# Performance work log

Hardware: AMD Instinct MI355X
Metric: run time of the kernel (lower is better)

Reference implementation:

```python
import jax, jax.numpy as jnp
import numpy as np

B, L = 8, 1024
VOCAB = 5000
DW = 256            # d_word_vec = d_model
H = 3 * DW          # hidden_size = 768
NH, HD = 12, 64     # n_head, d_k
D = NH * HD         # 768 = nhead*head_dim
D_INNER = 3072
N_LAYERS = 2
N_HIDDEN = 1024
N_OUT = 5000
MASK = 0
SCALE = 1.0 / float(np.sqrt(HD))


def _sinusoid(n_pos, d_hid):
    pos = np.arange(n_pos, dtype=np.float64)[:, None]
    hid = np.arange(d_hid)[None, :]
    tab = pos / np.power(10000.0, 2 * (hid // 2) / d_hid)
    tab[:, 0::2] = np.sin(tab[:, 0::2])
    tab[:, 1::2] = np.cos(tab[:, 1::2])
    tab[0] = 0.0  # padding_idx=0
    return jnp.asarray(tab, dtype=jnp.float32)


def _ln(x, g, b, eps=1e-5):
    mu = x.mean(-1, keepdims=True)
    var = ((x - mu) ** 2).mean(-1, keepdims=True)
    return (x - mu) * jax.lax.rsqrt(var + eps) * g + b


def _dense(x, w, b):
    # w: [out, in] (torch Conv 1x1 / Linear convention)
    return jnp.einsum('...i,oi->...o', x, w) + b


def _pwff(x, w1, b1, w2, b2, g, bn):
    out = _dense(jax.nn.relu(_dense(x, w1, b1)), w2, b2)
    return _ln(out + x, g, bn)


def _msa1(x, relay, wq, bq, wk, bk, wv, bv, wo, bo):
    # x: [B, L, H] nodes, relay: [B, H]. Star-Transformer ring attention:
    # window = 3 local neighbors + the relay node (4 keys per query).
    Bx, Lx, _ = x.shape
    q = _dense(x, wq, bq).reshape(Bx, Lx, NH, HD)
    k = _dense(x, wk, bk).reshape(Bx, Lx, NH, HD)
    v = _dense(x, wv, bv).reshape(Bx, Lx, NH, HD)
    kp = jnp.pad(k, ((0, 0), (1, 1), (0, 0), (0, 0)))
    vp = jnp.pad(v, ((0, 0), (1, 1), (0, 0), (0, 0)))
    k_win = jnp.stack([kp[:, u:u + Lx] for u in range(3)], axis=2)  # [B,L,3,NH,HD]
    v_win = jnp.stack([vp[:, u:u + Lx] for u in range(3)], axis=2)
    rk = _dense(relay, wk, bk).reshape(Bx, NH, HD)
    rv = _dense(relay, wv, bv).reshape(Bx, NH, HD)
    s_loc = jnp.einsum('blnh,blwnh->blwn', q, k_win)
    s_rel = jnp.einsum('blnh,bnh->bln', q, rk)
    scores = jnp.concatenate([s_loc, s_rel[:, :, None, :]], axis=2) * SCALE  # [B,L,4,NH]
    a = jax.nn.softmax(scores, axis=2)
    att = jnp.einsum('blwn,blwnh->blnh', a[:, :, :3], v_win) + a[:, :, 3][..., None] * rv[:, None]
    return _dense(att.reshape(Bx, Lx, D), wo, bo)


def _msa2(relay, nodes, smask, wq, bq, wk, bk, wv, bv, wo, bo):
    # Satellite->planet global attention: single query (relay) over [relay; nodes].
    Bx = relay.shape[0]
    y = jnp.concatenate([relay[:, None, :], nodes], axis=1)  # [B, 1+L, H]
    q = _dense(relay, wq, bq).reshape(Bx, NH, HD)
    k = _dense(y, wk, bk).reshape(Bx, -1, NH, HD)
    v = _dense(y, wv, bv).reshape(Bx, -1, NH, HD)
    pre = jnp.einsum('bnh,bsnh->bns', q, k) * SCALE
    pre = jnp.where(smask[:, None, :], -jnp.inf, pre)
    a = jax.nn.softmax(pre, axis=2)
    att = jnp.einsum('bns,bsnh->bnh', a, v).reshape(Bx, D)
    return _dense(att, wo, bo)


def setup_inputs():
    ks = iter(jax.random.split(jax.random.key(0), 40))
    def w(shape):
        return jax.random.normal(next(ks), shape, dtype=jnp.float32) * 0.02
    def z(shape):
        return jnp.zeros(shape, jnp.float32)
    def o(shape):
        return jnp.ones(shape, jnp.float32)
    inp = {}
    inp['src_seq'] = jax.random.randint(next(ks), (B, L, 3), 0, VOCAB, dtype=jnp.int32)
    inp['positions'] = jax.random.randint(next(ks), (B,), 0, L, dtype=jnp.int32)
    inp['emb'] = w((VOCAB, DW))
    inp['pos_table'] = _sinusoid(L, H)
    inp['norm_g'] = o((N_LAYERS, H)); inp['norm_b'] = z((N_LAYERS, H))
    inp['pw_w1'] = w((N_LAYERS, D_INNER, H)); inp['pw_b1'] = z((N_LAYERS, D_INNER))
    inp['pw_w2'] = w((N_LAYERS, H, D_INNER)); inp['pw_b2'] = z((N_LAYERS, H))
    inp['pw_g'] = o((N_LAYERS, H)); inp['pw_bn'] = z((N_LAYERS, H))
    for p in ['ring', 'star']:
        inp[p + '_wq'] = w((N_LAYERS, D, H)); inp[p + '_bq'] = z((N_LAYERS, D))
        inp[p + '_wk'] = w((N_LAYERS, D, H)); inp[p + '_bk'] = z((N_LAYERS, D))
        inp[p + '_wv'] = w((N_LAYERS, D, H)); inp[p + '_bv'] = z((N_LAYERS, D))
        inp[p + '_wo'] = w((N_LAYERS, H, D)); inp[p + '_bo'] = z((N_LAYERS, H))
    inp['head_w1'] = w((3, N_HIDDEN, 2 * H)); inp['head_b1'] = z((3, N_HIDDEN))
    inp['head_w2'] = w((3, N_OUT, N_HIDDEN)); inp['head_b2'] = z((3, N_OUT))
    return inp


def reference(src_seq, positions, emb, pos_table, norm_g, norm_b, pw_w1, pw_b1, pw_w2, pw_b2, pw_g, pw_bn, ring_wq, ring_bq, ring_wk, ring_bk, ring_wv, ring_bv, ring_wo, ring_bo, star_wq, star_bq, star_wk, star_bk, star_wv, star_bv, star_wo, star_bo, head_w1, head_b1, head_w2, head_b2):
    Bx, Lx, _ = src_seq.shape
    # [B,L,3,DW] -> [B,L,H], add (frozen) sinusoid positional encoding
    x = emb[src_seq].reshape(Bx, Lx, H) + pos_table[None, :Lx]
    mask_pad = src_seq[:, :, 0] == MASK               # True at padded positions
    smask = jnp.concatenate([jnp.zeros((Bx, 1), bool), mask_pad], axis=1)
    nodes = x
    relay = x.mean(axis=1)                            # [B, H]
    for i in range(N_LAYERS):
        h = _pwff(nodes, pw_w1[i], pw_b1[i], pw_w2[i], pw_b2[i], pw_g[i], pw_bn[i])
        ring = _msa1(h, relay, ring_wq[i], ring_bq[i], ring_wk[i], ring_bk[i], ring_wv[i], ring_bv[i], ring_wo[i], ring_bo[i])
        nodes = jax.nn.leaky_relu(_ln(ring, norm_g[i], norm_b[i]))
        relay = jax.nn.leaky_relu(_msa2(relay, nodes, smask, star_wq[i], star_bq[i], star_wk[i], star_bk[i], star_wv[i], star_bv[i], star_wo[i], star_bo[i]))
        nodes = jnp.where(mask_pad[:, :, None], 0.0, nodes)
    target = nodes[jnp.arange(Bx), positions]         # [B, H]
    ft = jnp.concatenate([relay, target], axis=1)     # [B, 2H]
    outs = [_dense(jax.nn.relu(_dense(ft, head_w1[j], head_b1[j])), head_w2[j], head_b2[j]) for j in range(3)]
    return jnp.concatenate(outs, axis=1).reshape(3 * Bx, N_OUT)
```

## Files before the change

kernel.cpp:

```cpp
#include <hip/hip_runtime.h>
#include <cstdint>
#include <cstddef>


typedef unsigned short u16;
typedef __attribute__((ext_vector_type(4))) float f32x4;
typedef __attribute__((ext_vector_type(8))) __bf16 bf16x8;

#define NB 8
#define SEQ 1024
#define HDIM 768
#define NHEAD 12
#define HD 64
#define DINNER 3072
#define NHID 1024
#define NOUT 5000
#define ATT_SCALE 0.125f

static __device__ __forceinline__ float b2f(u16 u) {
  union { float f; uint32_t i; } v; v.i = ((uint32_t)u) << 16; return v.f;
}
static __device__ __forceinline__ u16 f2b(float f) {
  union { float f; uint32_t i; } v; v.f = f;
  uint32_t r = v.i + 0x7fffu + ((v.i >> 16) & 1u);
  return (u16)(r >> 16);
}

static __device__ __forceinline__ void gl2lds16(const void* g, void* l) {
  __builtin_amdgcn_global_load_lds(
      (__attribute__((address_space(1))) void*)(uintptr_t)g,
      (__attribute__((address_space(3))) void*)l, 16, 0, 0);
}

static __device__ __forceinline__ float blk_sum(float v, float* red) {
  #pragma unroll
  for (int off = 32; off > 0; off >>= 1) v += __shfl_down(v, off, 64);
  if ((threadIdx.x & 63) == 0) red[threadIdx.x >> 6] = v;
  __syncthreads();
  float r = red[0] + red[1] + red[2] + red[3];
  __syncthreads();
  return r;
}
static __device__ __forceinline__ float blk_max(float v, float* red) {
  #pragma unroll
  for (int off = 32; off > 0; off >>= 1) v = fmaxf(v, __shfl_down(v, off, 64));
  if ((threadIdx.x & 63) == 0) red[threadIdx.x >> 6] = v;
  __syncthreads();
  float r = fmaxf(fmaxf(red[0], red[1]), fmaxf(red[2], red[3]));
  __syncthreads();
  return r;
}

struct Cvt4 {
  const float* s0; const float* s1; const float* s2; const float* s3;
  u16* d0; u16* d1; u16* d2; u16* d3;
  int c1, c2, c3, c4;
};
__global__ __launch_bounds__(256) void cvt4_k(Cvt4 a) {
  const int i = blockIdx.x * 256 + threadIdx.x;
  if (i >= a.c4) return;
  const float* s; u16* d; int j;
  if (i < a.c1)      { s = a.s0; d = a.d0; j = i; }
  else if (i < a.c2) { s = a.s1; d = a.d1; j = i - a.c1; }
  else if (i < a.c3) { s = a.s2; d = a.d2; j = i - a.c2; }
  else               { s = a.s3; d = a.d3; j = i - a.c3; }
  const float4 v = ((const float4*)s)[j];
  ushort4 o;
  o.x = f2b(v.x); o.y = f2b(v.y); o.z = f2b(v.z); o.w = f2b(v.w);
  ((ushort4*)d)[j] = o;
}

template <int ACT>
__global__ __launch_bounds__(256) void gemm_bt(
    const u16* __restrict__ A,
    const u16* W0, const u16* W1, const u16* W2,
    const float* b0, const float* b1, const float* b2,
    u16* C0, u16* C1, u16* C2,
    int M, int N, int K) {
  __shared__ u16 As[128 * 32];
  __shared__ u16 Bs[128 * 32];
  const int z = blockIdx.z;
  const u16* W = z == 0 ? W0 : (z == 1 ? W1 : W2);
  const float* bias = z == 0 ? b0 : (z == 1 ? b1 : b2);
  u16* C = z == 0 ? C0 : (z == 1 ? C1 : C2);

  const int tid  = threadIdx.x;
  const int wave = tid >> 6;
  const int lane = tid & 63;
  const int bm = blockIdx.y * 128;
  const int bn = blockIdx.x * 128;
  const int wrq = wave >> 1, wcq = wave & 1;
  const int r16 = lane & 15, quad = lane >> 4;
  const int srow = lane >> 2;
  const int scol = (lane & 3) << 3;

  f32x4 acc[4][4] = {};

  for (int k0 = 0; k0 < K; k0 += 32) {
    __syncthreads();
    #pragma unroll
    for (int t = 0; t < 2; ++t) {
      const int rowa = wave * 32 + t * 16;
      gl2lds16(A + (size_t)(bm + rowa + srow) * K + (k0 + scol), (char*)As + (rowa << 6));
      gl2lds16(W + (size_t)(bn + rowa + srow) * K + (k0 + scol), (char*)Bs + (rowa << 6));
    }
    __syncthreads();
    bf16x8 af[4], bf[4];
    #pragma unroll
    for (int i = 0; i < 4; ++i)
      af[i] = *reinterpret_cast<const bf16x8*>(&As[(wrq * 64 + i * 16 + r16) * 32 + quad * 8]);
    #pragma unroll
    for (int j = 0; j < 4; ++j)
      bf[j] = *reinterpret_cast<const bf16x8*>(&Bs[(wcq * 64 + j * 16 + r16) * 32 + quad * 8]);
    #pragma unroll
    for (int i = 0; i < 4; ++i)
      #pragma unroll
      for (int j = 0; j < 4; ++j)
        acc[i][j] = __builtin_amdgcn_mfma_f32_16x16x32_bf16(af[i], bf[j], acc[i][j], 0, 0, 0);
  }

  #pragma unroll
  for (int j = 0; j < 4; ++j) {
    const int n = bn + wcq * 64 + j * 16 + r16;
    const float bv = bias[n];
    #pragma unroll
    for (int i = 0; i < 4; ++i) {
      const int m0 = bm + wrq * 64 + i * 16 + quad * 4;
      #pragma unroll
      for (int r = 0; r < 4; ++r) {
        float vv = acc[i][j][r] + bv;
        if (ACT == 1) vv = fmaxf(vv, 0.0f);
        C[(size_t)(m0 + r) * N + n] = f2b(vv);
      }
    }
  }
}

__global__ __launch_bounds__(256) void embed_k(
    const int* __restrict__ src, const float* __restrict__ emb,
    const float* __restrict__ pt, float* __restrict__ x,
    u16* __restrict__ xb) {
  const int r = blockIdx.x;
  const int l = r & (SEQ - 1);
  const int tid = threadIdx.x;
  #pragma unroll
  for (int it = 0; it < 3; ++it) {
    const int idx = tid + it * 256;
    const int c = idx >> 8, d = idx & 255;
    const int tok = src[r * 3 + c];
    const float v = emb[(size_t)tok * 256 + d] + pt[(size_t)l * HDIM + idx];
    x[(size_t)r * HDIM + idx] = v;
    xb[(size_t)r * HDIM + idx] = f2b(v);
  }
}

__global__ __launch_bounds__(256) void relay_mean1_k(
    const float* __restrict__ x, float* __restrict__ part) {
  const int cg = blockIdx.x, seg = blockIdx.y, b = blockIdx.z;
  const int h = cg * 256 + threadIdx.x;
  float s = 0.f;
  const int l0 = seg * 64;
  for (int l = l0; l < l0 + 64; ++l) s += x[((size_t)b * SEQ + l) * HDIM + h];
  part[((size_t)b * 16 + seg) * HDIM + h] = s;
}
__global__ __launch_bounds__(256) void relay_mean2_k(
    const float* __restrict__ part, float* __restrict__ relay) {
  const int b = blockIdx.y;
  const int h = blockIdx.x * 256 + threadIdx.x;
  float s = 0.f;
  #pragma unroll
  for (int i = 0; i < 16; ++i) s += part[((size_t)b * 16 + i) * HDIM + h];
  relay[b * HDIM + h] = s * (1.0f / 1024.0f);
}

__global__ __launch_bounds__(256) void ln_resid_k(
    const u16* __restrict__ pre, const float* __restrict__ res,
    const float* __restrict__ g, const float* __restrict__ bb,
    u16* __restrict__ out) {
  __shared__ float red[4];
  const int r = blockIdx.x;
  const int tid = threadIdx.x;
  const size_t base = (size_t)r * HDIM;
  float v0 = b2f(pre[base + tid])       + res[base + tid];
  float v1 = b2f(pre[base + tid + 256]) + res[base + tid + 256];
  float v2 = b2f(pre[base + tid + 512]) + res[base + tid + 512];
  const float mu = blk_sum(v0 + v1 + v2, red) * (1.0f / 768.0f);
  v0 -= mu; v1 -= mu; v2 -= mu;
  const float var = blk_sum(v0 * v0 + v1 * v1 + v2 * v2, red) * (1.0f / 768.0f);
  const float rs = rsqrtf(var + 1e-5f);
  out[base + tid]       = f2b(v0 * rs * g[tid]       + bb[tid]);
  out[base + tid + 256] = f2b(v1 * rs * g[tid + 256] + bb[tid + 256]);
  out[base + tid + 512] = f2b(v2 * rs * g[tid + 512] + bb[tid + 512]);
}

__global__ __launch_bounds__(256) void ln_leaky_mask_k(
    const u16* __restrict__ pre, const float* __restrict__ g,
    const float* __restrict__ bb, const int* __restrict__ src,
    float* __restrict__ out, u16* __restrict__ outb) {
  __shared__ float red[4];
  const int r = blockIdx.x;
  const int tid = threadIdx.x;
  const size_t base = (size_t)r * HDIM;
  float v0 = b2f(pre[base + tid]);
  float v1 = b2f(pre[base + tid + 256]);
  float v2 = b2f(pre[base + tid + 512]);
  const float mu = blk_sum(v0 + v1 + v2, red) * (1.0f / 768.0f);
  v0 -= mu; v1 -= mu; v2 -= mu;
  const float var = blk_sum(v0 * v0 + v1 * v1 + v2 * v2, red) * (1.0f / 768.0f);
  const float rs = rsqrtf(var + 1e-5f);
  const bool masked = (src[r * 3] == 0);
  float y0 = v0 * rs * g[tid]       + bb[tid];
  float y1 = v1 * rs * g[tid + 256] + bb[tid + 256];
  float y2 = v2 * rs * g[tid + 512] + bb[tid + 512];
  y0 = y0 > 0.f ? y0 : 0.01f * y0;
  y1 = y1 > 0.f ? y1 : 0.01f * y1;
  y2 = y2 > 0.f ? y2 : 0.01f * y2;
  if (masked) { y0 = 0.f; y1 = 0.f; y2 = 0.f; }
  out[base + tid]       = y0;  outb[base + tid]       = f2b(y0);
  out[base + tid + 256] = y1;  outb[base + tid + 256] = f2b(y1);
  out[base + tid + 512] = y2;  outb[base + tid + 512] = f2b(y2);
}

__global__ __launch_bounds__(256) void ring_attn_k(
    const u16* __restrict__ q, const u16* __restrict__ k,
    const u16* __restrict__ v, const float* __restrict__ rk,
    const float* __restrict__ rv, u16* __restrict__ att) {
  __shared__ float qs[HDIM];
  __shared__ float aw[NHEAD][4];
  const int r = blockIdx.x;
  const int b = r >> 10, l = r & (SEQ - 1);
  const int tid = threadIdx.x;
  const size_t base = (size_t)r * HDIM;
  #pragma unroll
  for (int it = 0; it < 3; ++it) {
    const int idx = tid + it * 256;
    qs[idx] = b2f(q[base + idx]);
  }
  __syncthreads();
  if (tid < NHEAD * 4) {
    const int n = tid >> 2, w = tid & 3;
    float a = 0.f;
    if (w < 3) {
      const int ll = l - 1 + w;
      if (ll >= 0 && ll < SEQ) {
        const u16* kp = k + base + (size_t)(w - 1) * HDIM + n * HD;
        #pragma unroll
        for (int d = 0; d < HD; ++d) a += qs[n * HD + d] * b2f(kp[d]);
      }
    } else {
      const float* kp = rk + b * HDIM + n * HD;
      #pragma unroll
      for (int d = 0; d < HD; ++d) a += qs[n * HD + d] * kp[d];
    }
    aw[n][w] = a * ATT_SCALE;
  }
  __syncthreads();
  if (tid < NHEAD) {
    const float s0 = aw[tid][0], s1 = aw[tid][1], s2 = aw[tid][2], s3 = aw[tid][3];
    const float m = fmaxf(fmaxf(s0, s1), fmaxf(s2, s3));
    const float e0 = __expf(s0 - m), e1 = __expf(s1 - m);
    const float e2 = __expf(s2 - m), e3 = __expf(s3 - m);
    const float inv = 1.0f / (e0 + e1 + e2 + e3);
    aw[tid][0] = e0 * inv; aw[tid][1] = e1 * inv;
    aw[tid][2] = e2 * inv; aw[tid][3] = e3 * inv;
  }
  __syncthreads();
  #pragma unroll
  for (int it = 0; it < 3; ++it) {
    const int idx = tid + it * 256;
    const int n = idx >> 6;
    float acc = aw[n][3] * rv[b * HDIM + idx];
    if (l > 0)       acc += aw[n][0] * b2f(v[base - HDIM + idx]);
    acc += aw[n][1] * b2f(v[base + idx]);
    if (l < SEQ - 1) acc += aw[n][2] * b2f(v[base + HDIM + idx]);
    att[base + idx] = f2b(acc);
  }
}

__global__ __launch_bounds__(256) void msa2_attn_k(
    const float* __restrict__ q2, const float* __restrict__ rk2,
    const float* __restrict__ rv2, const u16* __restrict__ k2,
    const u16* __restrict__ v2, const int* __restrict__ src,
    float* __restrict__ att) {
  __shared__ float qs[HD];
  __shared__ float sc[SEQ + 1];
  __shared__ float red[4];
  const int bid = blockIdx.x;
  const int b = bid / NHEAD, n = bid % NHEAD;
  const int tid = threadIdx.x;
  const int hb = b * HDIM + n * HD;
  if (tid < HD) qs[tid] = q2[hb + tid];
  __syncthreads();
  float lmax = -1e30f;
  for (int s = tid; s <= SEQ; s += 256) {
    float sco;
    if (s == 0) {
      float a = 0.f;
      #pragma unroll
      for (int d = 0; d < HD; ++d) a += qs[d] * rk2[hb + d];
      sco = a * ATT_SCALE;
    } else {
      const int l = s - 1;
      if (src[(b * SEQ + l) * 3] == 0) {
        sco = -1e30f;
      } else {
        const u16* kp = k2 + ((size_t)b * SEQ + l) * HDIM + n * HD;
        float a = 0.f;
        #pragma unroll
        for (int d = 0; d < HD; ++d) a += qs[d] * b2f(kp[d]);
        sco = a * ATT_SCALE;
      }
    }
    sc[s] = sco;
    lmax = fmaxf(lmax, sco);
  }
  lmax = blk_max(lmax, red);
  float lsum = 0.f;
  for (int s = tid; s <= SEQ; s += 256) {
    const float e = __expf(sc[s] - lmax);
    sc[s] = e;
    lsum += e;
  }
  lsum = blk_sum(lsum, red);
  if (tid < HD) {
    const float inv = 1.0f / lsum;
    float acc = sc[0] * rv2[hb + tid];
    const u16* vp = v2 + (size_t)b * SEQ * HDIM + n * HD + tid;
    for (int l = 0; l < SEQ; ++l) acc += sc[l + 1] * b2f(vp[(size_t)l * HDIM]);
    att[hb + tid] = acc * inv;
  }
}

__global__ __launch_bounds__(256) void relay_proj_k(
    const float* __restrict__ A, int N, int nm,
    const float* W0, const float* W1, const float* W2,
    const float* b0, const float* b1, const float* b2v,
    float* O0, float* O1, float* O2, int act) {
  const int wid = blockIdx.x * 4 + (threadIdx.x >> 6);
  const int lane = threadIdx.x & 63;
  const int mat = wid / N, n = wid % N;
  const float* W  = mat == 0 ? W0 : (mat == 1 ? W1 : W2);
  const float* bb = mat == 0 ? b0 : (mat == 1 ? b1 : b2v);
  float* O        = mat == 0 ? O0 : (mat == 1 ? O1 : O2);
  const float4* wr = (const float4*)(W + (size_t)n * HDIM);
  float acc[NB] = {};
  #pragma unroll
  for (int it = 0; it < 3; ++it) {
    const int k4 = it * 64 + lane;
    const float4 wv = wr[k4];
    #pragma unroll
    for (int b = 0; b < NB; ++b) {
      const float4 av = *(const float4*)&A[b * HDIM + k4 * 4];
      acc[b] += av.x * wv.x + av.y * wv.y + av.z * wv.z + av.w * wv.w;
    }
  }
  #pragma unroll
  for (int b = 0; b < NB; ++b) {
    float a = acc[b];
    #pragma unroll
    for (int off = 32; off > 0; off >>= 1) a += __shfl_down(a, off, 64);
    if (lane == 0) {
      float v = a + bb[n];
      if (act == 2) v = v > 0.f ? v : 0.01f * v;
      O[(size_t)b * N + n] = v;
    }
  }
}

__global__ __launch_bounds__(256) void ft_k(
    const float* __restrict__ relay, const float* __restrict__ nodes,
    const int* __restrict__ positions, float* __restrict__ ft) {
  const int gid = blockIdx.x * 256 + threadIdx.x;
  const int b = gid / 1536, j = gid % 1536;
  if (j < HDIM) {
    ft[gid] = relay[b * HDIM + j];
  } else {
    const int p = positions[b];
    ft[gid] = nodes[((size_t)b * SEQ + p) * HDIM + (j - HDIM)];
  }
}

__global__ __launch_bounds__(256) void head1_k(
    const float* __restrict__ ft, const float* __restrict__ w,
    const float* __restrict__ bias, float* __restrict__ hid) {
  __shared__ float fs[NB * 1536];
  const int j = blockIdx.y;
  {
    const float4* s4 = (const float4*)ft;
    float4* d4 = (float4*)fs;
    for (int i = threadIdx.x; i < (NB * 1536) / 4; i += 256) d4[i] = s4[i];
  }
  __syncthreads();
  const int wave = threadIdx.x >> 6, lane = threadIdx.x & 63;
  const int o = blockIdx.x * 4 + wave;
  const float4* wr = (const float4*)(w + ((size_t)j * NHID + o) * 1536);
  float acc[NB] = {};
  #pragma unroll
  for (int it = 0; it < 6; ++it) {
    const int k4 = it * 64 + lane;
    const float4 wv = wr[k4];
    #pragma unroll
    for (int b = 0; b < NB; ++b) {
      const float4 hv = *(const float4*)&fs[b * 1536 + k4 * 4];
      acc[b] += hv.x * wv.x + hv.y * wv.y + hv.z * wv.z + hv.w * wv.w;
    }
  }
  #pragma unroll
  for (int b = 0; b < NB; ++b) {
    float a = acc[b];
    #pragma unroll
    for (int off = 32; off > 0; off >>= 1) a += __shfl_down(a, off, 64);
    if (lane == 0)
      hid[((size_t)j * NB + b) * NHID + o] = fmaxf(a + bias[j * NHID + o], 0.f);
  }
}

__global__ __launch_bounds__(256) void head2_k(
    const float* __restrict__ hid, const float* __restrict__ w,
    const float* __restrict__ bias, float* __restrict__ out) {
  __shared__ float hs[NB * NHID];
  const int j = blockIdx.y;
  {
    const float4* s4 = (const float4*)(hid + (size_t)j * NB * NHID);
    float4* d4 = (float4*)hs;
    for (int i = threadIdx.x; i < (NB * NHID) / 4; i += 256) d4[i] = s4[i];
  }
  __syncthreads();
  const int wave = threadIdx.x >> 6, lane = threadIdx.x & 63;
  const int o = blockIdx.x * 4 + wave;
  const float4* wr = (const float4*)(w + ((size_t)j * NOUT + o) * NHID);
  float acc[NB] = {};
  #pragma unroll
  for (int it = 0; it < 4; ++it) {
    const int k4 = it * 64 + lane;
    const float4 wv = wr[k4];
    #pragma unroll
    for (int b = 0; b < NB; ++b) {
      const float4 hv = *(const float4*)&hs[b * NHID + k4 * 4];
      acc[b] += hv.x * wv.x + hv.y * wv.y + hv.z * wv.z + hv.w * wv.w;
    }
  }
  #pragma unroll
  for (int b = 0; b < NB; ++b) {
    float a = acc[b];
    #pragma unroll
    for (int off = 32; off > 0; off >>= 1) a += __shfl_down(a, off, 64);
    if (lane == 0)
      out[(size_t)(b * 3 + j) * NOUT + o] = a + bias[j * NOUT + o];
  }
}

extern "C" void kernel_launch(void* const* d_in, const int* in_sizes, int n_in,
                              void* d_out, int out_size, void* d_ws, size_t ws_size,
                              hipStream_t stream) {
  (void)in_sizes; (void)n_in; (void)out_size; (void)ws_size;
  const int* src       = (const int*)d_in[0];
  const int* positions = (const int*)d_in[1];
  const float* emb   = (const float*)d_in[2];
  const float* pt    = (const float*)d_in[3];
  const float* norm_g = (const float*)d_in[4]; const float* norm_b = (const float*)d_in[5];
  const float* pw_w1 = (const float*)d_in[6];  const float* pw_b1 = (const float*)d_in[7];
  const float* pw_w2 = (const float*)d_in[8];  const float* pw_b2 = (const float*)d_in[9];
  const float* pw_g  = (const float*)d_in[10]; const float* pw_bn = (const float*)d_in[11];
  const float* ring_wq = (const float*)d_in[12]; const float* ring_bq = (const float*)d_in[13];
  const float* ring_wk = (const float*)d_in[14]; const float* ring_bk = (const float*)d_in[15];
  const float* ring_wv = (const float*)d_in[16]; const float* ring_bv = (const float*)d_in[17];
  const float* ring_wo = (const float*)d_in[18]; const float* ring_bo = (const float*)d_in[19];
  const float* star_wq = (const float*)d_in[20]; const float* star_bq = (const float*)d_in[21];
  const float* star_wk = (const float*)d_in[22]; const float* star_bk = (const float*)d_in[23];
  const float* star_wv = (const float*)d_in[24]; const float* star_bv = (const float*)d_in[25];
  const float* star_wo = (const float*)d_in[26]; const float* star_bo = (const float*)d_in[27];
  const float* head_w1 = (const float*)d_in[28]; const float* head_b1 = (const float*)d_in[29];
  const float* head_w2 = (const float*)d_in[30]; const float* head_b2 = (const float*)d_in[31];

  char* ws = (char*)d_ws;
  const size_t NTOK = (size_t)NB * SEQ * HDIM;
  float* nodes   = (float*)(ws);
  u16* preln     = (u16*)(ws + NTOK * 4);
  u16* cbase     = (u16*)(ws + NTOK * 6);
  u16* inner  = cbase;
  u16* slotC0 = cbase;
  u16* slotC1 = cbase + 1 * NTOK;
  u16* slotC2 = cbase + 2 * NTOK;
  u16* slotC3 = cbase + 3 * NTOK;
  u16* shared12  = (u16*)(ws + NTOK * 14);
  u16* wc        = (u16*)(ws + NTOK * 16);
  char* small    = ws + NTOK * 16 + 9437184;
  float* part  = (float*)(small);
  float* relay = (float*)(small + 393216);
  float* sb0 = (float*)(small + 393216 + 1 * 24576);
  float* sb1 = (float*)(small + 393216 + 2 * 24576);
  float* sb2 = (float*)(small + 393216 + 3 * 24576);
  float* sb3 = (float*)(small + 393216 + 4 * 24576);
  float* ftb = (float*)(small + 393216 + 5 * 24576);
  float* hid = (float*)(small + 393216 + 5 * 24576 + 49152);

  u16* nodes_b16 = shared12;
  u16* hbuf      = shared12;

  embed_k<<<NB * SEQ, 256, 0, stream>>>(src, emb, pt, nodes, nodes_b16);
  relay_mean1_k<<<dim3(3, 16, NB), 256, 0, stream>>>(nodes, part);
  relay_mean2_k<<<dim3(3, NB), 256, 0, stream>>>(part, relay);

  const int NW1 = DINNER * HDIM;
  const int NQK = HDIM * HDIM;

  for (int i = 0; i < 2; ++i) {
    const float* pw_w1_l = pw_w1 + (size_t)i * NW1;
    const float* pw_w2_l = pw_w2 + (size_t)i * NW1;
    const float* pw_b1_l = pw_b1 + (size_t)i * DINNER;
    const float* pw_b2_l = pw_b2 + (size_t)i * HDIM;
    const float* pw_g_l  = pw_g + (size_t)i * HDIM;
    const float* pw_bn_l = pw_bn + (size_t)i * HDIM;
    const float* ng_l = norm_g + (size_t)i * HDIM;
    const float* nb_l = norm_b + (size_t)i * HDIM;
    const float* rwq = ring_wq + (size_t)i * NQK; const float* rbq = ring_bq + (size_t)i * HDIM;
    const float* rwk = ring_wk + (size_t)i * NQK; const float* rbk = ring_bk + (size_t)i * HDIM;
    const float* rwv = ring_wv + (size_t)i * NQK; const float* rbv = ring_bv + (size_t)i * HDIM;
    const float* rwo = ring_wo + (size_t)i * NQK; const float* rbo = ring_bo + (size_t)i * HDIM;
    const float* swq = star_wq + (size_t)i * NQK; const float* sbq = star_bq + (size_t)i * HDIM;
    const float* swk = star_wk + (size_t)i * NQK; const float* sbk = star_bk + (size_t)i * HDIM;
    const float* swv = star_wv + (size_t)i * NQK; const float* sbv = star_bv + (size_t)i * HDIM;
    const float* swo = star_wo + (size_t)i * NQK; const float* sbo = star_bo + (size_t)i * HDIM;

    u16* wc_pw1 = wc;
    u16* wc_pw2 = wc + NW1;
    {
      Cvt4 a = { pw_w1_l, pw_w2_l, pw_w1_l, pw_w1_l,
                 wc_pw1, wc_pw2, wc_pw1, wc_pw1,
                 NW1 / 4, NW1 / 2, NW1 / 2, NW1 / 2 };
      cvt4_k<<<(NW1 / 2 + 255) / 256, 256, 0, stream>>>(a);
    }
    gemm_bt<1><<<dim3(DINNER / 128, 64, 1), 256, 0, stream>>>(
        nodes_b16, wc_pw1, wc_pw1, wc_pw1, pw_b1_l, pw_b1_l, pw_b1_l,
        inner, inner, inner, NB * SEQ, DINNER, HDIM);
    gemm_bt<0><<<dim3(HDIM / 128, 64, 1), 256, 0, stream>>>(
        inner, wc_pw2, wc_pw2, wc_pw2, pw_b2_l, pw_b2_l, pw_b2_l,
        preln, preln, preln, NB * SEQ, HDIM, DINNER);
    ln_resid_k<<<NB * SEQ, 256, 0, stream>>>(preln, nodes, pw_g_l, pw_bn_l, hbuf);

    u16* wc_rq = wc;
    u16* wc_rk = wc + NQK;
    u16* wc_rv = wc + 2 * NQK;
    u16* wc_ro = wc + 3 * NQK;
    {
      Cvt4 a = { rwq, rwk, rwv, rwo, wc_rq, wc_rk, wc_rv, wc_ro,
                 NQK / 4, NQK / 2, 3 * NQK / 4, NQK };
      cvt4_k<<<(NQK + 255) / 256, 256, 0, stream>>>(a);
    }
    gemm_bt<0><<<dim3(HDIM / 128, 64, 3), 256, 0, stream>>>(
        hbuf, wc_rq, wc_rk, wc_rv, rbq, rbk, rbv,
        slotC0, slotC1, slotC2, NB * SEQ, HDIM, HDIM);
    relay_proj_k<<<2 * HDIM / 4, 256, 0, stream>>>(
        relay, HDIM, 2, rwk, rwv, rwk, rbk, rbv, rbk, sb0, sb1, sb2, 0);
    ring_attn_k<<<NB * SEQ, 256, 0, stream>>>(slotC0, slotC1, slotC2, sb0, sb1, slotC3);
    gemm_bt<0><<<dim3(HDIM / 128, 64, 1), 256, 0, stream>>>(
        slotC3, wc_ro, wc_ro, wc_ro, rbo, rbo, rbo,
        preln, preln, preln, NB * SEQ, HDIM, HDIM);
    ln_leaky_mask_k<<<NB * SEQ, 256, 0, stream>>>(preln, ng_l, nb_l, src, nodes, nodes_b16);

    u16* wc_sk = wc;
    u16* wc_sv = wc + NQK;
    {
      Cvt4 a = { swk, swv, swk, swk, wc_sk, wc_sv, wc_sk, wc_sk,
                 NQK / 4, NQK / 2, NQK / 2, NQK / 2 };
      cvt4_k<<<(NQK / 2 + 255) / 256, 256, 0, stream>>>(a);
    }
    gemm_bt<0><<<dim3(HDIM / 128, 64, 2), 256, 0, stream>>>(
        nodes_b16, wc_sk, wc_sv, wc_sv, sbk, sbv, sbv,
        slotC0, slotC1, slotC1, NB * SEQ, HDIM, HDIM);
    relay_proj_k<<<3 * HDIM / 4, 256, 0, stream>>>(
        relay, HDIM, 3, swq, swk, swv, sbq, sbk, sbv, sb0, sb1, sb2, 0);
    msa2_attn_k<<<NB * NHEAD, 256, 0, stream>>>(sb0, sb1, sb2, slotC0, slotC1, src, sb3);
    relay_proj_k<<<HDIM / 4, 256, 0, stream>>>(
        sb3, HDIM, 1, swo, swo, swo, sbo, sbo, sbo, relay, sb1, sb2, 2);
  }

  ft_k<<<48, 256, 0, stream>>>(relay, nodes, positions, ftb);
  head1_k<<<dim3(NHID / 4, 3), 256, 0, stream>>>(ftb, head_w1, head_b1, hid);
  head2_k<<<dim3(NOUT / 4, 3), 256, 0, stream>>>(hid, head_w2, head_b2, (float*)d_out);
}
```

Before: 1.042 ms.

## Halve GEMM M-tile for N=768 GEMMs and parallelize ring and star attention dot products

Templates the bf16 GEMM on its M tile size and launches the N=768 GEMMs with 64-row tiles, doubling block count so the small grids (6x64) fill more compute units. The ring attention score computation now splits each 64-wide dot product across 4 lanes using vectorized 16-byte loads and a shuffle reduction. The star attention kernel uses vectorized key loads, and its value accumulation now spreads across all 4 waves instead of only 64 threads, followed by a shared-memory reduction. The smaller tile reduces operand reuse per block and adds more redundant weight loads.

```diff
diff --git a/kernel.cpp b/kernel.cpp
--- a/kernel.cpp
+++ b/kernel.cpp
@@ -24,6 +24,11 @@
   union { float f; uint32_t i; } v; v.f = f;
   uint32_t r = v.i + 0x7fffu + ((v.i >> 16) & 1u);
   return (u16)(r >> 16);
+}
+static __device__ __forceinline__ float2 b2f2(uint32_t u) {
+  union { float f; uint32_t i; } lo, hi;
+  lo.i = u << 16; hi.i = u & 0xffff0000u;
+  return make_float2(lo.f, hi.f);
 }
 
 static __device__ __forceinline__ void gl2lds16(const void* g, void* l) {
@@ -70,14 +75,15 @@
   ((ushort4*)d)[j] = o;
 }
 
-template <int ACT>
+template <int ACT, int TM>
 __global__ __launch_bounds__(256) void gemm_bt(
     const u16* __restrict__ A,
     const u16* W0, const u16* W1, const u16* W2,
     const float* b0, const float* b1, const float* b2,
     u16* C0, u16* C1, u16* C2,
     int M, int N, int K) {
-  __shared__ u16 As[128 * 32];
+  constexpr int MI = TM / 32;
+  __shared__ u16 As[TM * 32];
   __shared__ u16 Bs[128 * 32];
   const int z = blockIdx.z;
   const u16* W = z == 0 ? W0 : (z == 1 ? W1 : W2);
@@ -87,33 +93,37 @@
   const int tid  = threadIdx.x;
   const int wave = tid >> 6;
   const int lane = tid & 63;
-  const int bm = blockIdx.y * 128;
+  const int bm = blockIdx.y * TM;
   const int bn = blockIdx.x * 128;
   const int wrq = wave >> 1, wcq = wave & 1;
   const int r16 = lane & 15, quad = lane >> 4;
   const int srow = lane >> 2;
   const int scol = (lane & 3) << 3;
 
-  f32x4 acc[4][4] = {};
+  f32x4 acc[MI][4] = {};
 
   for (int k0 = 0; k0 < K; k0 += 32) {
     __syncthreads();
     #pragma unroll
+    for (int t = 0; t < TM / 64; ++t) {
+      const int rowa = wave * (TM / 4) + t * 16;
+      gl2lds16(A + (size_t)(bm + rowa + srow) * K + (k0 + scol), (char*)As + (rowa << 6));
+    }
+    #pragma unroll
     for (int t = 0; t < 2; ++t) {
-      const int rowa = wave * 32 + t * 16;
-      gl2lds16(A + (size_t)(bm + rowa + srow) * K + (k0 + scol), (char*)As + (rowa << 6));
-      gl2lds16(W + (size_t)(bn + rowa + srow) * K + (k0 + scol), (char*)Bs + (rowa << 6));
+      const int rowb = wave * 32 + t * 16;
+      gl2lds16(W + (size_t)(bn + rowb + srow) * K + (k0 + scol), (char*)Bs + (rowb << 6));
     }
     __syncthreads();
-    bf16x8 af[4], bf[4];
-    #pragma unroll
-    for (int i = 0; i < 4; ++i)
-      af[i] = *reinterpret_cast<const bf16x8*>(&As[(wrq * 64 + i * 16 + r16) * 32 + quad * 8]);
+    bf16x8 af[MI], bf[4];
+    #pragma unroll
+    for (int i = 0; i < MI; ++i)
+      af[i] = *reinterpret_cast<const bf16x8*>(&As[(wrq * (TM / 2) + i * 16 + r16) * 32 + quad * 8]);
     #pragma unroll
     for (int j = 0; j < 4; ++j)
       bf[j] = *reinterpret_cast<const bf16x8*>(&Bs[(wcq * 64 + j * 16 + r16) * 32 + quad * 8]);
     #pragma unroll
-    for (int i = 0; i < 4; ++i)
+    for (int i = 0; i < MI; ++i)
       #pragma unroll
       for (int j = 0; j < 4; ++j)
         acc[i][j] = __builtin_amdgcn_mfma_f32_16x16x32_bf16(af[i], bf[j], acc[i][j], 0, 0, 0);
@@ -124,8 +134,8 @@
     const int n = bn + wcq * 64 + j * 16 + r16;
     const float bv = bias[n];
     #pragma unroll
-    for (int i = 0; i < 4; ++i) {
-      const int m0 = bm + wrq * 64 + i * 16 + quad * 4;
+    for (int i = 0; i < MI; ++i) {
+      const int m0 = bm + wrq * (TM / 2) + i * 16 + quad * 4;
       #pragma unroll
       for (int r = 0; r < 4; ++r) {
         float vv = acc[i][j][r] + bv;
@@ -237,22 +247,39 @@
     qs[idx] = b2f(q[base + idx]);
   }
   __syncthreads();
-  if (tid < NHEAD * 4) {
-    const int n = tid >> 2, w = tid & 3;
+  if (tid < 192) {
+    const int u_ = tid >> 2;
+    const int l4 = tid & 3;
+    const int n = u_ >> 2, w = u_ & 3;
+    const float* qrow = qs + n * HD + l4 * 16;
     float a = 0.f;
     if (w < 3) {
       const int ll = l - 1 + w;
       if (ll >= 0 && ll < SEQ) {
-        const u16* kp = k + base + (size_t)(w - 1) * HDIM + n * HD;
+        const uint4* kp4 =
+            (const uint4*)(k + base + (size_t)(w - 1) * HDIM + n * HD + l4 * 16);
         #pragma unroll
-        for (int d = 0; d < HD; ++d) a += qs[n * HD + d] * b2f(kp[d]);
+        for (int t = 0; t < 2; ++t) {
+          const uint4 u = kp4[t];
+          const float2 f0 = b2f2(u.x), f1 = b2f2(u.y);
+          const float2 f2_ = b2f2(u.z), f3 = b2f2(u.w);
+          const float* q8 = qrow + t * 8;
+          a += q8[0] * f0.x + q8[1] * f0.y + q8[2] * f1.x + q8[3] * f1.y
+             + q8[4] * f2_.x + q8[5] * f2_.y + q8[6] * f3.x + q8[7] * f3.y;
+        }
       }
     } else {
-      const float* kp = rk + b * HDIM + n * HD;
+      const float4* kp4 = (const float4*)(rk + b * HDIM + n * HD + l4 * 16);
       #pragma unroll
-      for (int d = 0; d < HD; ++d) a += qs[n * HD + d] * kp[d];
-    }
-    aw[n][w] = a * ATT_SCALE;
+      for (int t = 0; t < 4; ++t) {
+        const float4 kv = kp4[t];
+        const float* q4 = qrow + t * 4;
+        a += q4[0] * kv.x + q4[1] * kv.y + q4[2] * kv.z + q4[3] * kv.w;
+      }
+    }
+    a += __shfl_xor(a, 1, 4);
+    a += __shfl_xor(a, 2, 4);
+    if (l4 == 0) aw[n][w] = a * ATT_SCALE;
   }
   __syncthreads();
   if (tid < NHEAD) {
@@ -285,6 +312,7 @@
   __shared__ float qs[HD];
   __shared__ float sc[SEQ + 1];
   __shared__ float red[4];
+  __shared__ float vred[4][HD];
   const int bid = blockIdx.x;
   const int b = bid / NHEAD, n = bid % NHEAD;
   const int tid = threadIdx.x;
@@ -304,10 +332,18 @@
       if (src[(b * SEQ + l) * 3] == 0) {
         sco = -1e30f;
       } else {
-        const u16* kp = k2 + ((size_t)b * SEQ + l) * HDIM + n * HD;
+        const uint4* kp4 =
+            (const uint4*)(k2 + ((size_t)b * SEQ + l) * HDIM + n * HD);
         float a = 0.f;
         #pragma unroll
-        for (int d = 0; d < HD; ++d) a += qs[d] * b2f(kp[d]);
+        for (int t = 0; t < 8; ++t) {
+          const uint4 u = kp4[t];
+          const float2 f0 = b2f2(u.x), f1 = b2f2(u.y);
+          const float2 f2_ = b2f2(u.z), f3 = b2f2(u.w);
+          const float* q8 = qs + t * 8;
+          a += q8[0] * f0.x + q8[1] * f0.y + q8[2] * f1.x + q8[3] * f1.y
+             + q8[4] * f2_.x + q8[5] * f2_.y + q8[6] * f3.x + q8[7] * f3.y;
+        }
         sco = a * ATT_SCALE;
       }
     }
@@ -322,12 +358,20 @@
     lsum += e;
   }
   lsum = blk_sum(lsum, red);
+  {
+    const int dd = tid & 63, grp = tid >> 6;
+    float acc = 0.f;
+    const u16* vp = v2 + (size_t)b * SEQ * HDIM + n * HD + dd;
+    for (int l = grp; l < SEQ; l += 4)
+      acc += sc[l + 1] * b2f(vp[(size_t)l * HDIM]);
+    vred[grp][dd] = acc;
+  }
+  __syncthreads();
   if (tid < HD) {
     const float inv = 1.0f / lsum;
-    float acc = sc[0] * rv2[hb + tid];
-    const u16* vp = v2 + (size_t)b * SEQ * HDIM + n * HD + tid;
-    for (int l = 0; l < SEQ; ++l) acc += sc[l + 1] * b2f(vp[(size_t)l * HDIM]);
-    att[hb + tid] = acc * inv;
+    const float a = sc[0] * rv2[hb + tid]
+                  + vred[0][tid] + vred[1][tid] + vred[2][tid] + vred[3][tid];
+    att[hb + tid] = a * inv;
   }
 }
 
@@ -531,10 +575,10 @@
                  NW1 / 4, NW1 / 2, NW1 / 2, NW1 / 2 };
       cvt4_k<<<(NW1 / 2 + 255) / 256, 256, 0, stream>>>(a);
     }
-    gemm_bt<1><<<dim3(DINNER / 128, 64, 1), 256, 0, stream>>>(
+    gemm_bt<1, 128><<<dim3(DINNER / 128, 64, 1), 256, 0, stream>>>(
         nodes_b16, wc_pw1, wc_pw1, wc_pw1, pw_b1_l, pw_b1_l, pw_b1_l,
         inner, inner, inner, NB * SEQ, DINNER, HDIM);
-    gemm_bt<0><<<dim3(HDIM / 128, 64, 1), 256, 0, stream>>>(
+    gemm_bt<0, 64><<<dim3(HDIM / 128, 128, 1), 256, 0, stream>>>(
         inner, wc_pw2, wc_pw2, wc_pw2, pw_b2_l, pw_b2_l, pw_b2_l,
         preln, preln, preln, NB * SEQ, HDIM, DINNER);
     ln_resid_k<<<NB * SEQ, 256, 0, stream>>>(preln, nodes, pw_g_l, pw_bn_l, hbuf);
@@ -548,13 +592,13 @@
                  NQK / 4, NQK / 2, 3 * NQK / 4, NQK };
       cvt4_k<<<(NQK + 255) / 256, 256, 0, stream>>>(a);
     }
-    gemm_bt<0><<<dim3(HDIM / 128, 64, 3), 256, 0, stream>>>(
+    gemm_bt<0, 64><<<dim3(HDIM / 128, 128, 3), 256, 0, stream>>>(
         hbuf, wc_rq, wc_rk, wc_rv, rbq, rbk, rbv,
         slotC0, slotC1, slotC2, NB * SEQ, HDIM, HDIM);
     relay_proj_k<<<2 * HDIM / 4, 256, 0, stream>>>(
         relay, HDIM, 2, rwk, rwv, rwk, rbk, rbv, rbk, sb0, sb1, sb2, 0);
     ring_attn_k<<<NB * SEQ, 256, 0, stream>>>(slotC0, slotC1, slotC2, sb0, sb1, slotC3);
-    gemm_bt<0><<<dim3(HDIM / 128, 64, 1), 256, 0, stream>>>(
+    gemm_bt<0, 64><<<dim3(HDIM / 128, 128, 1), 256, 0, stream>>>(
         slotC3, wc_ro, wc_ro, wc_ro, rbo, rbo, rbo,
         preln, preln, preln, NB * SEQ, HDIM, HDIM);
     ln_leaky_mask_k<<<NB * SEQ, 256, 0, stream>>>(preln, ng_l, nb_l, src, nodes, nodes_b16);
@@ -566,7 +610,7 @@
                  NQK / 4, NQK / 2, NQK / 2, NQK / 2 };
       cvt4_k<<<(NQK / 2 + 255) / 256, 256, 0, stream>>>(a);
     }
-    gemm_bt<0><<<dim3(HDIM / 128, 64, 2), 256, 0, stream>>>(
+    gemm_bt<0, 64><<<dim3(HDIM / 128, 128, 2), 256, 0, stream>>>(
         nodes_b16, wc_sk, wc_sv, wc_sv, sbk, sbv, sbv,
         slotC0, slotC1, slotC1, NB * SEQ, HDIM, HDIM);
     relay_proj_k<<<3 * HDIM / 4, 256, 0, stream>>>(
```

Result: slower. 1.090 ms (+4.6%).
